# Optimization experiments

Hardware: AMD Instinct MI355X
Metric: run time of the kernel (lower is better)

The kernel has to match this reference:

```python
import jax, jax.numpy as jnp
import numpy as np

WINDOW = 128
LOOK_BACK = 1
LOOK_FWD = 0   # causal=True -> look_forward defaults to 0
DIM = 64       # rotary dim == head dim


def look_around(x, backward=LOOK_BACK, forward=LOOK_FWD, pad_value=-1):
    # x: [b, windows, window, ...]; pad along windows axis, concat along axis 2
    w = x.shape[1]
    pad = [(0, 0), (backward, forward)] + [(0, 0)] * (x.ndim - 2)
    px = jnp.pad(x, pad, constant_values=pad_value)
    return jnp.concatenate([px[:, i:i + w] for i in range(forward + backward + 1)], axis=2)


def rotate_half(x):
    h = (x.shape[-1] + 1) // 2  # ceil split, matches torch .split([ceil, floor])
    x1, x2 = x[..., :h], x[..., h:]
    return jnp.concatenate([-x2, x1], axis=-1)


def setup_inputs() -> dict:
    key = jax.random.key(0)
    kq, kk, kv = jax.random.split(key, 3)
    shape = (4, 16, 4096, 64)
    return {
        "q": jax.random.normal(kq, shape, dtype=jnp.float32),
        "k": jax.random.normal(kk, shape, dtype=jnp.float32),
        "v": jax.random.normal(kv, shape, dtype=jnp.float32),
    }


def reference(q, k, v):
    B, H, T, e = q.shape
    b = B * H
    q, k, v = (t.reshape(b, T, e) for t in (q, k, v))

    # sinusoidal rotary embeddings (start_pos = 0)
    inv_freq = 1.0 / (10000.0 ** (jnp.arange(0, DIM, 2, dtype=jnp.float32) / DIM))
    t_idx = jnp.arange(T, dtype=jnp.float32)
    freqs = jnp.einsum('i,j->ij', t_idx, inv_freq)          # [T, DIM/2]
    emb = jnp.concatenate([freqs, freqs], axis=-1)[:, :DIM][None]  # [1, T, DIM]
    cos, sin = jnp.cos(emb), jnp.sin(emb)
    q = q * cos + rotate_half(q) * sin
    k = k * cos + rotate_half(k) * sin

    # T is a multiple of WINDOW so autopad is a no-op
    w = T // WINDOW
    bq, bk, bv = (t.reshape(b, w, WINDOW, e) for t in (q, k, v))
    bk = look_around(bk)   # [b, w, (LB+LF+1)*WINDOW, e], padded with -1 (masked below)
    bv = look_around(bv)

    b_t = jnp.arange(T).reshape(1, w, WINDOW)
    bq_t = b_t
    bq_k = look_around(b_t)  # [1, w, (LB+LF+1)*WINDOW]

    dots = (jnp.einsum('bwie,bwje->bwij', bq.astype(jnp.float32), bk.astype(jnp.float32))
            * (e ** -0.5)).astype(q.dtype)
    mask_value = -jnp.finfo(dots.dtype).max

    # causal mask (exact_windowsize=False)
    causal_mask = bq_t[:, :, :, None] < bq_k[:, :, None, :]
    dots = jnp.where(causal_mask, mask_value, dots)
    # look-around padding mask
    dots = jnp.where((bq_k == -1)[:, :, None, :], mask_value, dots)

    attn = jax.nn.softmax(dots, axis=-1)
    out = jnp.einsum('bwij,bwje->bwie', attn, bv)
    return out.reshape(B, H, T, e)
```

## Files before the change

### kernel.cpp

```cpp
#include <hip/hip_runtime.h>
#include <hip/hip_bf16.h>

#define T_LEN 4096
#define DHEAD 64
#define WINSZ 128
#define NWIN 32
#define NBH 64
#define NWPB 4
#define NGRP (NWIN / NWPB)
#define FLTMAX 3.402823466e38f

typedef float f32x4 __attribute__((ext_vector_type(4)));
typedef short s16x8 __attribute__((ext_vector_type(8)));
typedef short s16x4 __attribute__((ext_vector_type(4)));

__device__ __forceinline__ unsigned short f2b(float x) {
  return __builtin_bit_cast(unsigned short, __float2bfloat16(x));
}

__global__ void rope_tab_kernel(float* __restrict__ tab) {
  const int idx = blockIdx.x * 256 + threadIdx.x;
  if (idx >= T_LEN * 32) return;
  const int t = idx >> 5;
  const int i = idx & 31;
  const float freq = powf(10000.0f, -(float)i / 32.0f);
  float s, c;
  sincosf((float)t * freq, &s, &c);
  tab[idx] = c;
  tab[T_LEN * 32 + idx] = s;
}

__global__ __launch_bounds__(512, 4) void lattn_kernel(
    const float* __restrict__ qg, const float* __restrict__ kg,
    const float* __restrict__ vg, const float* __restrict__ tab,
    float* __restrict__ outg) {
  __shared__ __align__(16) unsigned short Kh[2][WINSZ * DHEAD];
  __shared__ __align__(16) unsigned short Vh[2][DHEAD * WINSZ];

  const int bid = blockIdx.x;
  const int grp = bid & (NGRP - 1);
  const int bh  = bid >> 3;
  const int tid = threadIdx.x;
  const int lane = tid & 63;
  const int wv = tid >> 6;
  const int l15 = lane & 15;
  const int g = lane >> 4;

  const size_t base = (size_t)bh * T_LEN * DHEAD;
  const int win0 = grp * NWPB;
  const bool use_tab = (tab != nullptr);
  const float* ct = tab;
  const float* st = tab + T_LEN * 32;

  auto stage_half = [&](int hb, int kb) {
    {
      const int c = tid & 7;
      const int rr = tid >> 3;
      #pragma unroll
      for (int p = 0; p < 2; ++p) {
        const int kr = p * 64 + rr;
        const int kt = kb + kr;
        float xa[4] = {0.f,0.f,0.f,0.f}, xb[4] = {0.f,0.f,0.f,0.f};
        float cs[4] = {1.f,1.f,1.f,1.f}, sn[4] = {0.f,0.f,0.f,0.f};
        if (kt >= 0) {
          const float* kp = kg + base + (size_t)kt * DHEAD + 4 * c;
          *(float4*)xa = *(const float4*)kp;
          *(float4*)xb = *(const float4*)(kp + 32);
          if (use_tab) {
            *(float4*)cs = *(const float4*)(ct + kt * 32 + 4 * c);
            *(float4*)sn = *(const float4*)(st + kt * 32 + 4 * c);
          } else {
            #pragma unroll
            for (int j = 0; j < 4; ++j) {
              const float f = powf(10000.0f, -(float)(4 * c + j) / 32.0f);
              sincosf((float)kt * f, &sn[j], &cs[j]);
            }
          }
        }
        unsigned wlo[2], whi[2];
        #pragma unroll
        for (int h = 0; h < 2; ++h) {
          const int j0 = 2 * h, j1 = 2 * h + 1;
          wlo[h] = (unsigned)f2b(xa[j0]*cs[j0] - xb[j0]*sn[j0]) |
                   ((unsigned)f2b(xa[j1]*cs[j1] - xb[j1]*sn[j1]) << 16);
          whi[h] = (unsigned)f2b(xb[j0]*cs[j0] + xa[j0]*sn[j0]) |
                   ((unsigned)f2b(xb[j1]*cs[j1] + xa[j1]*sn[j1]) << 16);
        }
        const int su = (kr & 7) << 3;
        *(uint2*)&Kh[hb][kr * 64 + ((4 * c) ^ su)] = uint2{wlo[0], wlo[1]};
        *(uint2*)&Kh[hb][kr * 64 + ((4 * c + 32) ^ su)] = uint2{whi[0], whi[1]};
      }
    }
    {
      const int c = tid & 15;
      const int rp = tid >> 4;
      #pragma unroll
      for (int p = 0; p < 2; ++p) {
        const int kr = (p * 32 + rp) * 2;
        const int kt = kb + kr;
        float va[4] = {0.f,0.f,0.f,0.f}, vb[4] = {0.f,0.f,0.f,0.f};
        if (kt >= 0)
          *(float4*)va = *(const float4*)(vg + base + (size_t)kt * DHEAD + 4 * c);
        if (kt + 1 >= 0)
          *(float4*)vb = *(const float4*)(vg + base + (size_t)(kt + 1) * DHEAD + 4 * c);
        #pragma unroll
        for (int j = 0; j < 4; ++j) {
          const int d = 4 * c + j;
          const unsigned val = (unsigned)f2b(va[j]) | ((unsigned)f2b(vb[j]) << 16);
          *(unsigned*)&Vh[hb][d * WINSZ + (kr ^ ((d & 15) << 3))] = val;
        }
      }
    }
  };

  stage_half(0, win0 * WINSZ - WINSZ);
  stage_half(1, win0 * WINSZ);

  #pragma unroll 1
  for (int t = 0; t < NWPB; ++t) {
    const int win = win0 + t;
    const int q0 = win * WINSZ;
    const int pb = t & 1, ob = (t + 1) & 1;

    s16x8 qa0, qa1;
    {
      const int qrow = q0 + wv * 16 + l15;
      const float* qp = qg + base + (size_t)qrow * DHEAD + 8 * g;
      float xa[8], xb[8], cs[8], sn[8];
      *(float4*)&xa[0] = *(const float4*)qp;
      *(float4*)&xa[4] = *(const float4*)(qp + 4);
      *(float4*)&xb[0] = *(const float4*)(qp + 32);
      *(float4*)&xb[4] = *(const float4*)(qp + 36);
      if (use_tab) {
        const float* cp = ct + qrow * 32 + 8 * g;
        const float* sp = st + qrow * 32 + 8 * g;
        *(float4*)&cs[0] = *(const float4*)cp;
        *(float4*)&cs[4] = *(const float4*)(cp + 4);
        *(float4*)&sn[0] = *(const float4*)sp;
        *(float4*)&sn[4] = *(const float4*)(sp + 4);
      } else {
        #pragma unroll
        for (int j = 0; j < 8; ++j) {
          const float f = powf(10000.0f, -(float)(8 * g + j) / 32.0f);
          sincosf((float)qrow * f, &sn[j], &cs[j]);
        }
      }
      #pragma unroll
      for (int j = 0; j < 8; ++j) {
        qa0[j] = (short)f2b(xa[j]*cs[j] - xb[j]*sn[j]);
        qa1[j] = (short)f2b(xb[j]*cs[j] + xa[j]*sn[j]);
      }
    }

    __syncthreads();

    s16x8 pa[8];
    float inv;
    {
      f32x4 acc[16];
      #pragma unroll
      for (int nt = 0; nt < 16; ++nt) acc[nt] = f32x4{0.f, 0.f, 0.f, 0.f};
      #pragma unroll
      for (int nt = 0; nt < 16; ++nt) {
        const int hb = (nt < 8) ? pb : ob;
        const int krh = (nt & 7) * 16 + l15;
        const int su = (krh & 7) << 3;
        const s16x8 k0f = *(const s16x8*)&Kh[hb][krh * 64 + ((8 * g) ^ su)];
        const s16x8 k1f = *(const s16x8*)&Kh[hb][krh * 64 + ((8 * g + 32) ^ su)];
        acc[nt] = __builtin_amdgcn_mfma_f32_16x16x32_bf16(k0f, qa0, acc[nt], 0, 0, 0);
        acc[nt] = __builtin_amdgcn_mfma_f32_16x16x32_bf16(k1f, qa1, acc[nt], 0, 0, 0);
      }
      const int qloc = wv * 16 + l15;
      float mx = -FLTMAX;
      #pragma unroll
      for (int nt = 0; nt < 16; ++nt) {
        const bool pad = (win == 0) && (nt < 8);
        #pragma unroll
        for (int r = 0; r < 4; ++r) {
          const int kloc = nt * 16 + 4 * g + r;
          const bool msk = pad || (kloc > WINSZ + qloc);
          const float s = msk ? -FLTMAX : acc[nt][r];
          acc[nt][r] = s;
          mx = fmaxf(mx, s);
        }
      }
      mx = fmaxf(mx, __shfl_xor(mx, 16));
      mx = fmaxf(mx, __shfl_xor(mx, 32));
      float den = 0.f;
      #pragma unroll
      for (int nt = 0; nt < 16; ++nt) {
        #pragma unroll
        for (int r = 0; r < 4; ++r) {
          const float pv = __expf(0.125f * (acc[nt][r] - mx));
          acc[nt][r] = pv;
          den += pv;
        }
      }
      den += __shfl_xor(den, 16);
      den += __shfl_xor(den, 32);
      inv = 1.0f / den;
      #pragma unroll
      for (int ks = 0; ks < 8; ++ks) {
        #pragma unroll
        for (int j = 0; j < 4; ++j) {
          pa[ks][j]     = (short)f2b(acc[2 * ks][j]);
          pa[ks][j + 4] = (short)f2b(acc[2 * ks + 1][j]);
        }
      }
    }

    f32x4 oacc[4];
    #pragma unroll
    for (int nt = 0; nt < 4; ++nt) oacc[nt] = f32x4{0.f, 0.f, 0.f, 0.f};
    #pragma unroll
    for (int ks = 0; ks < 8; ++ks) {
      const int hb = (ks < 4) ? pb : ob;
      const int c1 = (ks & 3) * 32 + 4 * g;
      #pragma unroll
      for (int nt = 0; nt < 4; ++nt) {
        const int d = nt * 16 + l15;
        const int su = (d & 15) << 3;
        const s16x4 v0 = *(const s16x4*)&Vh[hb][d * WINSZ + (c1 ^ su)];
        const s16x4 v1 = *(const s16x4*)&Vh[hb][d * WINSZ + ((c1 + 16) ^ su)];
        const s16x8 vb = __builtin_shufflevector(v0, v1, 0, 1, 2, 3, 4, 5, 6, 7);
        oacc[nt] = __builtin_amdgcn_mfma_f32_16x16x32_bf16(pa[ks], vb, oacc[nt], 0, 0, 0);
      }
    }

    float* op = outg + base;
    #pragma unroll
    for (int r = 0; r < 4; ++r) {
      const float ir = __shfl(inv, 4 * g + r, 64);
      const int qrow = q0 + wv * 16 + 4 * g + r;
      #pragma unroll
      for (int nt = 0; nt < 4; ++nt)
        op[(size_t)qrow * DHEAD + nt * 16 + l15] = oacc[nt][r] * ir;
    }

    if (t + 1 < NWPB) {
      __syncthreads();
      stage_half(t & 1, (win + 1) * WINSZ);
    }
  }
}

extern "C" void kernel_launch(void* const* d_in, const int* in_sizes, int n_in,
                              void* d_out, int out_size, void* d_ws, size_t ws_size,
                              hipStream_t stream) {
  (void)in_sizes; (void)n_in; (void)out_size;
  const float* q = (const float*)d_in[0];
  const float* k = (const float*)d_in[1];
  const float* v = (const float*)d_in[2];
  float* out = (float*)d_out;

  float* tab = nullptr;
  const size_t tab_bytes = (size_t)2 * T_LEN * 32 * sizeof(float);
  if (ws_size >= tab_bytes) {
    tab = (float*)d_ws;
    rope_tab_kernel<<<dim3((T_LEN * 32 + 255) / 256), dim3(256), 0, stream>>>(tab);
  }
  lattn_kernel<<<dim3(NBH * NGRP), dim3(512), 0, stream>>>(q, k, v, tab, out);
}
```

Baseline: 253.7 us.

## Precompute rotated bf16 K/V in workspace and DMA them into LDS per window

Adds a prep kernel that applies rotary embedding to K, converts K and V to swizzled bf16 (V transposed) in a workspace buffer. The attention kernel then runs one window per block and copies K/V tiles straight into LDS with global_load_lds, removing the per-block fp32 load and convert work. The block index is remapped across the grid, and a single-pass fallback kernel handles the case where the workspace is too small. The trade-off is an extra kernel launch and a full extra write and read of bf16 K/V through global memory, in exchange for less fp32 traffic and less compute inside the attention kernel.

```diff
diff --git a/kernel.cpp b/kernel.cpp
--- a/kernel.cpp
+++ b/kernel.cpp
@@ -6,8 +6,6 @@
 #define WINSZ 128
 #define NWIN 32
 #define NBH 64
-#define NWPB 4
-#define NGRP (NWIN / NWPB)
 #define FLTMAX 3.402823466e38f
 
 typedef float f32x4 __attribute__((ext_vector_type(4)));
@@ -16,6 +14,12 @@
 
 __device__ __forceinline__ unsigned short f2b(float x) {
   return __builtin_bit_cast(unsigned short, __float2bfloat16(x));
+}
+
+__device__ __forceinline__ void dma16(const void* g, void* l) {
+  __builtin_amdgcn_global_load_lds(
+      (const __attribute__((address_space(1))) void*)g,
+      (__attribute__((address_space(3))) void*)l, 16, 0, 0);
 }
 
 __global__ void rope_tab_kernel(float* __restrict__ tab) {
@@ -30,16 +34,78 @@
   tab[T_LEN * 32 + idx] = s;
 }
 
-__global__ __launch_bounds__(512, 4) void lattn_kernel(
-    const float* __restrict__ qg, const float* __restrict__ kg,
-    const float* __restrict__ vg, const float* __restrict__ tab,
+__global__ __launch_bounds__(512, 4) void kv_prep_kernel(
+    const float* __restrict__ kg, const float* __restrict__ vg,
+    const float* __restrict__ tab,
+    unsigned short* __restrict__ Kp, unsigned short* __restrict__ Vp) {
+  const int bid = blockIdx.x;
+  const int chunk = bid & 31;
+  const int bh = bid >> 5;
+  const int tid = threadIdx.x;
+  const int kb = chunk * WINSZ;
+  const size_t base = (size_t)bh * T_LEN * DHEAD;
+  const float* ct = tab;
+  const float* st = tab + T_LEN * 32;
+
+  {
+    const int c = tid & 7;
+    const int rr = tid >> 3;
+    #pragma unroll
+    for (int p = 0; p < 2; ++p) {
+      const int kt = kb + p * 64 + rr;
+      const float* kp = kg + base + (size_t)kt * DHEAD + 4 * c;
+      float xa[4], xb[4], cs[4], sn[4];
+      *(float4*)xa = *(const float4*)kp;
+      *(float4*)xb = *(const float4*)(kp + 32);
+      *(float4*)cs = *(const float4*)(ct + kt * 32 + 4 * c);
+      *(float4*)sn = *(const float4*)(st + kt * 32 + 4 * c);
+      unsigned wlo[2], whi[2];
+      #pragma unroll
+      for (int h = 0; h < 2; ++h) {
+        const int j0 = 2 * h, j1 = 2 * h + 1;
+        wlo[h] = (unsigned)f2b(xa[j0]*cs[j0] - xb[j0]*sn[j0]) |
+                 ((unsigned)f2b(xa[j1]*cs[j1] - xb[j1]*sn[j1]) << 16);
+        whi[h] = (unsigned)f2b(xb[j0]*cs[j0] + xa[j0]*sn[j0]) |
+                 ((unsigned)f2b(xb[j1]*cs[j1] + xa[j1]*sn[j1]) << 16);
+      }
+      const int su = (kt & 7) << 3;
+      unsigned short* krow = Kp + base + (size_t)kt * DHEAD;
+      *(uint2*)&krow[(4 * c) ^ su] = uint2{wlo[0], wlo[1]};
+      *(uint2*)&krow[(4 * c + 32) ^ su] = uint2{whi[0], whi[1]};
+    }
+  }
+  {
+    const int c = tid & 15;
+    const int rp = tid >> 4;
+    unsigned short* vb_base = Vp + (size_t)bh * DHEAD * T_LEN;
+    #pragma unroll
+    for (int p = 0; p < 2; ++p) {
+      const int kr = (p * 32 + rp) * 2;
+      const int kt = kb + kr;
+      float va[4], vb[4];
+      *(float4*)va = *(const float4*)(vg + base + (size_t)kt * DHEAD + 4 * c);
+      *(float4*)vb = *(const float4*)(vg + base + (size_t)(kt + 1) * DHEAD + 4 * c);
+      #pragma unroll
+      for (int j = 0; j < 4; ++j) {
+        const int d = 4 * c + j;
+        const unsigned val = (unsigned)f2b(va[j]) | ((unsigned)f2b(vb[j]) << 16);
+        *(unsigned*)&vb_base[(size_t)d * T_LEN + kb + (kr ^ ((d & 15) << 3))] = val;
+      }
+    }
+  }
+}
+
+__global__ __launch_bounds__(512, 4) void lattn2_kernel(
+    const float* __restrict__ qg, const unsigned short* __restrict__ Kp,
+    const unsigned short* __restrict__ Vp, const float* __restrict__ tab,
     float* __restrict__ outg) {
   __shared__ __align__(16) unsigned short Kh[2][WINSZ * DHEAD];
   __shared__ __align__(16) unsigned short Vh[2][DHEAD * WINSZ];
 
-  const int bid = blockIdx.x;
-  const int grp = bid & (NGRP - 1);
-  const int bh  = bid >> 3;
+  const int H = blockIdx.x;
+  const int L = (H & 7) * 256 + (H >> 3);
+  const int win = L & (NWIN - 1);
+  const int bh  = L >> 5;
   const int tid = threadIdx.x;
   const int lane = tid & 63;
   const int wv = tid >> 6;
@@ -47,200 +113,335 @@
   const int g = lane >> 4;
 
   const size_t base = (size_t)bh * T_LEN * DHEAD;
-  const int win0 = grp * NWPB;
+  const int q0 = win * WINSZ;
+  const float* ct = tab;
+  const float* st = tab + T_LEN * 32;
+
+  {
+    const unsigned short* gk = Kp + base + (size_t)q0 * DHEAD;
+    const unsigned short* gv = Vp + (size_t)bh * DHEAD * T_LEN;
+    #pragma unroll
+    for (int i = 0; i < 2; ++i) {
+      const int idx = (wv * 2 + i) * 512 + lane * 8;
+      dma16(gk + idx, &Kh[1][idx]);
+      const int ch = wv * 2 + i;
+      const int d = ch * 4 + (lane >> 4);
+      const int col = (lane & 15) * 8;
+      dma16(gv + (size_t)d * T_LEN + q0 + col, &Vh[1][ch * 512 + lane * 8]);
+    }
+    if (win > 0) {
+      const unsigned short* gkp = Kp + base + (size_t)(q0 - WINSZ) * DHEAD;
+      #pragma unroll
+      for (int i = 0; i < 2; ++i) {
+        const int idx = (wv * 2 + i) * 512 + lane * 8;
+        dma16(gkp + idx, &Kh[0][idx]);
+        const int ch = wv * 2 + i;
+        const int d = ch * 4 + (lane >> 4);
+        const int col = (lane & 15) * 8;
+        dma16(gv + (size_t)d * T_LEN + (q0 - WINSZ) + col, &Vh[0][ch * 512 + lane * 8]);
+      }
+    } else {
+      #pragma unroll
+      for (int i = 0; i < 2; ++i) {
+        *(uint4*)&Kh[0][tid * 16 + i * 8] = uint4{0u, 0u, 0u, 0u};
+        *(uint4*)&Vh[0][tid * 16 + i * 8] = uint4{0u, 0u, 0u, 0u};
+      }
+    }
+  }
+
+  s16x8 qa0, qa1;
+  {
+    const int qrow = q0 + wv * 16 + l15;
+    const float* qp = qg + base + (size_t)qrow * DHEAD + 8 * g;
+    float xa[8], xb[8], cs[8], sn[8];
+    *(float4*)&xa[0] = *(const float4*)qp;
+    *(float4*)&xa[4] = *(const float4*)(qp + 4);
+    *(float4*)&xb[0] = *(const float4*)(qp + 32);
+    *(float4*)&xb[4] = *(const float4*)(qp + 36);
+    const float* cp = ct + qrow * 32 + 8 * g;
+    const float* sp = st + qrow * 32 + 8 * g;
+    *(float4*)&cs[0] = *(const float4*)cp;
+    *(float4*)&cs[4] = *(const float4*)(cp + 4);
+    *(float4*)&sn[0] = *(const float4*)sp;
+    *(float4*)&sn[4] = *(const float4*)(sp + 4);
+    #pragma unroll
+    for (int j = 0; j < 8; ++j) {
+      qa0[j] = (short)f2b(xa[j]*cs[j] - xb[j]*sn[j]);
+      qa1[j] = (short)f2b(xb[j]*cs[j] + xa[j]*sn[j]);
+    }
+  }
+
+  __syncthreads();
+
+  s16x8 pa[8];
+  float inv;
+  {
+    f32x4 acc[16];
+    #pragma unroll
+    for (int nt = 0; nt < 16; ++nt) acc[nt] = f32x4{0.f, 0.f, 0.f, 0.f};
+    #pragma unroll
+    for (int nt = 0; nt < 16; ++nt) {
+      const int hb = nt >> 3;
+      const int krh = (nt & 7) * 16 + l15;
+      const int su = (krh & 7) << 3;
+      const s16x8 k0f = *(const s16x8*)&Kh[hb][krh * 64 + ((8 * g) ^ su)];
+      const s16x8 k1f = *(const s16x8*)&Kh[hb][krh * 64 + ((8 * g + 32) ^ su)];
+      acc[nt] = __builtin_amdgcn_mfma_f32_16x16x32_bf16(k0f, qa0, acc[nt], 0, 0, 0);
+      acc[nt] = __builtin_amdgcn_mfma_f32_16x16x32_bf16(k1f, qa1, acc[nt], 0, 0, 0);
+    }
+    const int qloc = wv * 16 + l15;
+    float mx = -FLTMAX;
+    #pragma unroll
+    for (int nt = 0; nt < 16; ++nt) {
+      const bool pad = (win == 0) && (nt < 8);
+      #pragma unroll
+      for (int r = 0; r < 4; ++r) {
+        const int kloc = nt * 16 + 4 * g + r;
+        const bool msk = pad || (kloc > WINSZ + qloc);
+        const float s = msk ? -FLTMAX : acc[nt][r];
+        acc[nt][r] = s;
+        mx = fmaxf(mx, s);
+      }
+    }
+    mx = fmaxf(mx, __shfl_xor(mx, 16));
+    mx = fmaxf(mx, __shfl_xor(mx, 32));
+    float den = 0.f;
+    #pragma unroll
+    for (int nt = 0; nt < 16; ++nt) {
+      #pragma unroll
+      for (int r = 0; r < 4; ++r) {
+        const float pv = __expf(0.125f * (acc[nt][r] - mx));
+        acc[nt][r] = pv;
+        den += pv;
+      }
+    }
+    den += __shfl_xor(den, 16);
+    den += __shfl_xor(den, 32);
+    inv = 1.0f / den;
+    #pragma unroll
+    for (int ks = 0; ks < 8; ++ks) {
+      #pragma unroll
+      for (int j = 0; j < 4; ++j) {
+        pa[ks][j]     = (short)f2b(acc[2 * ks][j]);
+        pa[ks][j + 4] = (short)f2b(acc[2 * ks + 1][j]);
+      }
+    }
+  }
+
+  f32x4 oacc[4];
+  #pragma unroll
+  for (int nt = 0; nt < 4; ++nt) oacc[nt] = f32x4{0.f, 0.f, 0.f, 0.f};
+  #pragma unroll
+  for (int ks = 0; ks < 8; ++ks) {
+    const int hb = ks >> 2;
+    const int c1 = (ks & 3) * 32 + 4 * g;
+    #pragma unroll
+    for (int nt = 0; nt < 4; ++nt) {
+      const int d = nt * 16 + l15;
+      const int su = (d & 15) << 3;
+      const s16x4 v0 = *(const s16x4*)&Vh[hb][d * WINSZ + (c1 ^ su)];
+      const s16x4 v1 = *(const s16x4*)&Vh[hb][d * WINSZ + ((c1 + 16) ^ su)];
+      const s16x8 vb = __builtin_shufflevector(v0, v1, 0, 1, 2, 3, 4, 5, 6, 7);
+      oacc[nt] = __builtin_amdgcn_mfma_f32_16x16x32_bf16(pa[ks], vb, oacc[nt], 0, 0, 0);
+    }
+  }
+
+  float* op = outg + base;
+  #pragma unroll
+  for (int r = 0; r < 4; ++r) {
+    const float ir = __shfl(inv, 4 * g + r, 64);
+    const int qrow = q0 + wv * 16 + 4 * g + r;
+    #pragma unroll
+    for (int nt = 0; nt < 4; ++nt)
+      op[(size_t)qrow * DHEAD + nt * 16 + l15] = oacc[nt][r] * ir;
+  }
+}
+
+__global__ __launch_bounds__(512, 4) void lattn_fb_kernel(
+    const float* __restrict__ qg, const float* __restrict__ kg,
+    const float* __restrict__ vg, const float* __restrict__ tab,
+    float* __restrict__ outg) {
+  __shared__ __align__(16) unsigned short Kl[256 * DHEAD];
+  __shared__ __align__(16) unsigned short Vt[DHEAD * 256];
+  const int bid = blockIdx.x;
+  const int win = bid & (NWIN - 1);
+  const int bh  = bid >> 5;
+  const int tid = threadIdx.x;
+  const int lane = tid & 63;
+  const int wv = tid >> 6;
+  const int l15 = lane & 15;
+  const int g = lane >> 4;
+  const size_t base = (size_t)bh * T_LEN * DHEAD;
+  const int q0 = win * WINSZ;
+  const int k0 = q0 - WINSZ;
   const bool use_tab = (tab != nullptr);
   const float* ct = tab;
   const float* st = tab + T_LEN * 32;
-
-  auto stage_half = [&](int hb, int kb) {
-    {
-      const int c = tid & 7;
-      const int rr = tid >> 3;
-      #pragma unroll
-      for (int p = 0; p < 2; ++p) {
-        const int kr = p * 64 + rr;
-        const int kt = kb + kr;
-        float xa[4] = {0.f,0.f,0.f,0.f}, xb[4] = {0.f,0.f,0.f,0.f};
-        float cs[4] = {1.f,1.f,1.f,1.f}, sn[4] = {0.f,0.f,0.f,0.f};
-        if (kt >= 0) {
-          const float* kp = kg + base + (size_t)kt * DHEAD + 4 * c;
-          *(float4*)xa = *(const float4*)kp;
-          *(float4*)xb = *(const float4*)(kp + 32);
-          if (use_tab) {
-            *(float4*)cs = *(const float4*)(ct + kt * 32 + 4 * c);
-            *(float4*)sn = *(const float4*)(st + kt * 32 + 4 * c);
-          } else {
-            #pragma unroll
-            for (int j = 0; j < 4; ++j) {
-              const float f = powf(10000.0f, -(float)(4 * c + j) / 32.0f);
-              sincosf((float)kt * f, &sn[j], &cs[j]);
-            }
+  {
+    const int c = tid & 7;
+    const int rr = tid >> 3;
+    #pragma unroll
+    for (int p = 0; p < 4; ++p) {
+      const int kr = p * 64 + rr;
+      const int kt = k0 + kr;
+      float xa[4] = {0.f,0.f,0.f,0.f}, xb[4] = {0.f,0.f,0.f,0.f};
+      float cs[4] = {1.f,1.f,1.f,1.f}, sn[4] = {0.f,0.f,0.f,0.f};
+      if (kt >= 0) {
+        const float* kp = kg + base + (size_t)kt * DHEAD + 4 * c;
+        *(float4*)xa = *(const float4*)kp;
+        *(float4*)xb = *(const float4*)(kp + 32);
+        if (use_tab) {
+          *(float4*)cs = *(const float4*)(ct + kt * 32 + 4 * c);
+          *(float4*)sn = *(const float4*)(st + kt * 32 + 4 * c);
+        } else {
+          #pragma unroll
+          for (int j = 0; j < 4; ++j) {
+            const float f = powf(10000.0f, -(float)(4 * c + j) / 32.0f);
+            sincosf((float)kt * f, &sn[j], &cs[j]);
           }
         }
-        unsigned wlo[2], whi[2];
-        #pragma unroll
-        for (int h = 0; h < 2; ++h) {
-          const int j0 = 2 * h, j1 = 2 * h + 1;
-          wlo[h] = (unsigned)f2b(xa[j0]*cs[j0] - xb[j0]*sn[j0]) |
-                   ((unsigned)f2b(xa[j1]*cs[j1] - xb[j1]*sn[j1]) << 16);
-          whi[h] = (unsigned)f2b(xb[j0]*cs[j0] + xa[j0]*sn[j0]) |
-                   ((unsigned)f2b(xb[j1]*cs[j1] + xa[j1]*sn[j1]) << 16);
-        }
-        const int su = (kr & 7) << 3;
-        *(uint2*)&Kh[hb][kr * 64 + ((4 * c) ^ su)] = uint2{wlo[0], wlo[1]};
-        *(uint2*)&Kh[hb][kr * 64 + ((4 * c + 32) ^ su)] = uint2{whi[0], whi[1]};
-      }
-    }
-    {
-      const int c = tid & 15;
-      const int rp = tid >> 4;
-      #pragma unroll
-      for (int p = 0; p < 2; ++p) {
-        const int kr = (p * 32 + rp) * 2;
-        const int kt = kb + kr;
-        float va[4] = {0.f,0.f,0.f,0.f}, vb[4] = {0.f,0.f,0.f,0.f};
-        if (kt >= 0)
-          *(float4*)va = *(const float4*)(vg + base + (size_t)kt * DHEAD + 4 * c);
-        if (kt + 1 >= 0)
-          *(float4*)vb = *(const float4*)(vg + base + (size_t)(kt + 1) * DHEAD + 4 * c);
-        #pragma unroll
-        for (int j = 0; j < 4; ++j) {
-          const int d = 4 * c + j;
-          const unsigned val = (unsigned)f2b(va[j]) | ((unsigned)f2b(vb[j]) << 16);
-          *(unsigned*)&Vh[hb][d * WINSZ + (kr ^ ((d & 15) << 3))] = val;
-        }
-      }
-    }
-  };
-
-  stage_half(0, win0 * WINSZ - WINSZ);
-  stage_half(1, win0 * WINSZ);
-
-  #pragma unroll 1
-  for (int t = 0; t < NWPB; ++t) {
-    const int win = win0 + t;
-    const int q0 = win * WINSZ;
-    const int pb = t & 1, ob = (t + 1) & 1;
-
-    s16x8 qa0, qa1;
-    {
-      const int qrow = q0 + wv * 16 + l15;
-      const float* qp = qg + base + (size_t)qrow * DHEAD + 8 * g;
-      float xa[8], xb[8], cs[8], sn[8];
-      *(float4*)&xa[0] = *(const float4*)qp;
-      *(float4*)&xa[4] = *(const float4*)(qp + 4);
-      *(float4*)&xb[0] = *(const float4*)(qp + 32);
-      *(float4*)&xb[4] = *(const float4*)(qp + 36);
-      if (use_tab) {
-        const float* cp = ct + qrow * 32 + 8 * g;
-        const float* sp = st + qrow * 32 + 8 * g;
-        *(float4*)&cs[0] = *(const float4*)cp;
-        *(float4*)&cs[4] = *(const float4*)(cp + 4);
-        *(float4*)&sn[0] = *(const float4*)sp;
-        *(float4*)&sn[4] = *(const float4*)(sp + 4);
-      } else {
-        #pragma unroll
-        for (int j = 0; j < 8; ++j) {
-          const float f = powf(10000.0f, -(float)(8 * g + j) / 32.0f);
-          sincosf((float)qrow * f, &sn[j], &cs[j]);
-        }
-      }
+      }
+      unsigned wlo[2], whi[2];
+      #pragma unroll
+      for (int h = 0; h < 2; ++h) {
+        const int j0 = 2 * h, j1 = 2 * h + 1;
+        wlo[h] = (unsigned)f2b(xa[j0]*cs[j0] - xb[j0]*sn[j0]) |
+                 ((unsigned)f2b(xa[j1]*cs[j1] - xb[j1]*sn[j1]) << 16);
+        whi[h] = (unsigned)f2b(xb[j0]*cs[j0] + xa[j0]*sn[j0]) |
+                 ((unsigned)f2b(xb[j1]*cs[j1] + xa[j1]*sn[j1]) << 16);
+      }
+      const int su = (kr & 7) << 3;
+      *(uint2*)&Kl[kr * 64 + ((4 * c) ^ su)] = uint2{wlo[0], wlo[1]};
+      *(uint2*)&Kl[kr * 64 + ((4 * c + 32) ^ su)] = uint2{whi[0], whi[1]};
+    }
+  }
+  {
+    const int c = tid & 15;
+    const int rp = tid >> 4;
+    #pragma unroll
+    for (int p = 0; p < 4; ++p) {
+      const int kr = (p * 32 + rp) * 2;
+      const int kt = k0 + kr;
+      float va[4] = {0.f,0.f,0.f,0.f}, vb[4] = {0.f,0.f,0.f,0.f};
+      if (kt >= 0)
+        *(float4*)va = *(const float4*)(vg + base + (size_t)kt * DHEAD + 4 * c);
+      if (kt + 1 >= 0)
+        *(float4*)vb = *(const float4*)(vg + base + (size_t)(kt + 1) * DHEAD + 4 * c);
+      #pragma unroll
+      for (int j = 0; j < 4; ++j) {
+        const int d = 4 * c + j;
+        const unsigned val = (unsigned)f2b(va[j]) | ((unsigned)f2b(vb[j]) << 16);
+        *(unsigned*)&Vt[d * 256 + (kr ^ ((d & 7) << 3))] = val;
+      }
+    }
+  }
+  s16x8 qa0, qa1;
+  {
+    const int qrow = q0 + wv * 16 + l15;
+    const float* qp = qg + base + (size_t)qrow * DHEAD + 8 * g;
+    float xa[8], xb[8], cs[8], sn[8];
+    *(float4*)&xa[0] = *(const float4*)qp;
+    *(float4*)&xa[4] = *(const float4*)(qp + 4);
+    *(float4*)&xb[0] = *(const float4*)(qp + 32);
+    *(float4*)&xb[4] = *(const float4*)(qp + 36);
+    if (use_tab) {
+      const float* cp = ct + qrow * 32 + 8 * g;
+      const float* sp = st + qrow * 32 + 8 * g;
+      *(float4*)&cs[0] = *(const float4*)cp;
+      *(float4*)&cs[4] = *(const float4*)(cp + 4);
+      *(float4*)&sn[0] = *(const float4*)sp;
+      *(float4*)&sn[4] = *(const float4*)(sp + 4);
+    } else {
       #pragma unroll
       for (int j = 0; j < 8; ++j) {
-        qa0[j] = (short)f2b(xa[j]*cs[j] - xb[j]*sn[j]);
-        qa1[j] = (short)f2b(xb[j]*cs[j] + xa[j]*sn[j]);
-      }
-    }
-
-    __syncthreads();
-
-    s16x8 pa[8];
-    float inv;
-    {
-      f32x4 acc[16];
-      #pragma unroll
-      for (int nt = 0; nt < 16; ++nt) acc[nt] = f32x4{0.f, 0.f, 0.f, 0.f};
-      #pragma unroll
-      for (int nt = 0; nt < 16; ++nt) {
-        const int hb = (nt < 8) ? pb : ob;
-        const int krh = (nt & 7) * 16 + l15;
-        const int su = (krh & 7) << 3;
-        const s16x8 k0f = *(const s16x8*)&Kh[hb][krh * 64 + ((8 * g) ^ su)];
-        const s16x8 k1f = *(const s16x8*)&Kh[hb][krh * 64 + ((8 * g + 32) ^ su)];
-        acc[nt] = __builtin_amdgcn_mfma_f32_16x16x32_bf16(k0f, qa0, acc[nt], 0, 0, 0);
-        acc[nt] = __builtin_amdgcn_mfma_f32_16x16x32_bf16(k1f, qa1, acc[nt], 0, 0, 0);
-      }
-      const int qloc = wv * 16 + l15;
-      float mx = -FLTMAX;
-      #pragma unroll
-      for (int nt = 0; nt < 16; ++nt) {
-        const bool pad = (win == 0) && (nt < 8);
-        #pragma unroll
-        for (int r = 0; r < 4; ++r) {
-          const int kloc = nt * 16 + 4 * g + r;
-          const bool msk = pad || (kloc > WINSZ + qloc);
-          const float s = msk ? -FLTMAX : acc[nt][r];
-          acc[nt][r] = s;
-          mx = fmaxf(mx, s);
-        }
-      }
-      mx = fmaxf(mx, __shfl_xor(mx, 16));
-      mx = fmaxf(mx, __shfl_xor(mx, 32));
-      float den = 0.f;
-      #pragma unroll
-      for (int nt = 0; nt < 16; ++nt) {
-        #pragma unroll
-        for (int r = 0; r < 4; ++r) {
-          const float pv = __expf(0.125f * (acc[nt][r] - mx));
-          acc[nt][r] = pv;
-          den += pv;
-        }
-      }
-      den += __shfl_xor(den, 16);
-      den += __shfl_xor(den, 32);
-      inv = 1.0f / den;
-      #pragma unroll
-      for (int ks = 0; ks < 8; ++ks) {
-        #pragma unroll
-        for (int j = 0; j < 4; ++j) {
-          pa[ks][j]     = (short)f2b(acc[2 * ks][j]);
-          pa[ks][j + 4] = (short)f2b(acc[2 * ks + 1][j]);
-        }
-      }
-    }
-
-    f32x4 oacc[4];
-    #pragma unroll
-    for (int nt = 0; nt < 4; ++nt) oacc[nt] = f32x4{0.f, 0.f, 0.f, 0.f};
+        const float f = powf(10000.0f, -(float)(8 * g + j) / 32.0f);
+        sincosf((float)qrow * f, &sn[j], &cs[j]);
+      }
+    }
+    #pragma unroll
+    for (int j = 0; j < 8; ++j) {
+      qa0[j] = (short)f2b(xa[j]*cs[j] - xb[j]*sn[j]);
+      qa1[j] = (short)f2b(xb[j]*cs[j] + xa[j]*sn[j]);
+    }
+  }
+  __syncthreads();
+  s16x8 pa[8];
+  float inv;
+  {
+    f32x4 acc[16];
+    #pragma unroll
+    for (int nt = 0; nt < 16; ++nt) acc[nt] = f32x4{0.f, 0.f, 0.f, 0.f};
+    #pragma unroll
+    for (int nt = 0; nt < 16; ++nt) {
+      const int krow = nt * 16 + l15;
+      const int su = (krow & 7) << 3;
+      const s16x8 k0f = *(const s16x8*)&Kl[krow * 64 + ((8 * g) ^ su)];
+      const s16x8 k1f = *(const s16x8*)&Kl[krow * 64 + ((8 * g + 32) ^ su)];
+      acc[nt] = __builtin_amdgcn_mfma_f32_16x16x32_bf16(k0f, qa0, acc[nt], 0, 0, 0);
+      acc[nt] = __builtin_amdgcn_mfma_f32_16x16x32_bf16(k1f, qa1, acc[nt], 0, 0, 0);
+    }
+    const int qloc = wv * 16 + l15;
+    float mx = -FLTMAX;
+    #pragma unroll
+    for (int nt = 0; nt < 16; ++nt) {
+      const bool pad = (win == 0) && (nt < 8);
+      #pragma unroll
+      for (int r = 0; r < 4; ++r) {
+        const int kloc = nt * 16 + 4 * g + r;
+        const bool msk = pad || (kloc > WINSZ + qloc);
+        const float s = msk ? -FLTMAX : acc[nt][r];
+        acc[nt][r] = s;
+        mx = fmaxf(mx, s);
+      }
+    }
+    mx = fmaxf(mx, __shfl_xor(mx, 16));
+    mx = fmaxf(mx, __shfl_xor(mx, 32));
+    float den = 0.f;
+    #pragma unroll
+    for (int nt = 0; nt < 16; ++nt) {
+      #pragma unroll
+      for (int r = 0; r < 4; ++r) {
+        const float pv = __expf(0.125f * (acc[nt][r] - mx));
+        acc[nt][r] = pv;
+        den += pv;
+      }
+    }
+    den += __shfl_xor(den, 16);
+    den += __shfl_xor(den, 32);
+    inv = 1.0f / den;
     #pragma unroll
     for (int ks = 0; ks < 8; ++ks) {
-      const int hb = (ks < 4) ? pb : ob;
-      const int c1 = (ks & 3) * 32 + 4 * g;
-      #pragma unroll
-      for (int nt = 0; nt < 4; ++nt) {
-        const int d = nt * 16 + l15;
-        const int su = (d & 15) << 3;
-        const s16x4 v0 = *(const s16x4*)&Vh[hb][d * WINSZ + (c1 ^ su)];
-        const s16x4 v1 = *(const s16x4*)&Vh[hb][d * WINSZ + ((c1 + 16) ^ su)];
-        const s16x8 vb = __builtin_shufflevector(v0, v1, 0, 1, 2, 3, 4, 5, 6, 7);
-        oacc[nt] = __builtin_amdgcn_mfma_f32_16x16x32_bf16(pa[ks], vb, oacc[nt], 0, 0, 0);
-      }
-    }
-
-    float* op = outg + base;
-    #pragma unroll
-    for (int r = 0; r < 4; ++r) {
-      const float ir = __shfl(inv, 4 * g + r, 64);
-      const int qrow = q0 + wv * 16 + 4 * g + r;
-      #pragma unroll
-      for (int nt = 0; nt < 4; ++nt)
-        op[(size_t)qrow * DHEAD + nt * 16 + l15] = oacc[nt][r] * ir;
-    }
-
-    if (t + 1 < NWPB) {
-      __syncthreads();
-      stage_half(t & 1, (win + 1) * WINSZ);
-    }
+      #pragma unroll
+      for (int j = 0; j < 4; ++j) {
+        pa[ks][j]     = (short)f2b(acc[2 * ks][j]);
+        pa[ks][j + 4] = (short)f2b(acc[2 * ks + 1][j]);
+      }
+    }
+  }
+  f32x4 oacc[4];
+  #pragma unroll
+  for (int nt = 0; nt < 4; ++nt) oacc[nt] = f32x4{0.f, 0.f, 0.f, 0.f};
+  #pragma unroll
+  for (int ks = 0; ks < 8; ++ks) {
+    #pragma unroll
+    for (int nt = 0; nt < 4; ++nt) {
+      const int d = nt * 16 + l15;
+      const int su = (d & 7) << 3;
+      const int c1 = ks * 32 + 4 * g;
+      const s16x4 v0 = *(const s16x4*)&Vt[d * 256 + (c1 ^ su)];
+      const s16x4 v1 = *(const s16x4*)&Vt[d * 256 + ((c1 + 16) ^ su)];
+      const s16x8 vb = __builtin_shufflevector(v0, v1, 0, 1, 2, 3, 4, 5, 6, 7);
+      oacc[nt] = __builtin_amdgcn_mfma_f32_16x16x32_bf16(pa[ks], vb, oacc[nt], 0, 0, 0);
+    }
+  }
+  float* op = outg + base;
+  #pragma unroll
+  for (int r = 0; r < 4; ++r) {
+    const float ir = __shfl(inv, 4 * g + r, 64);
+    const int qrow = q0 + wv * 16 + 4 * g + r;
+    #pragma unroll
+    for (int nt = 0; nt < 4; ++nt)
+      op[(size_t)qrow * DHEAD + nt * 16 + l15] = oacc[nt][r] * ir;
   }
 }
 
@@ -253,11 +454,22 @@
   const float* v = (const float*)d_in[2];
   float* out = (float*)d_out;
 
-  float* tab = nullptr;
   const size_t tab_bytes = (size_t)2 * T_LEN * 32 * sizeof(float);
-  if (ws_size >= tab_bytes) {
-    tab = (float*)d_ws;
+  const size_t kp_bytes  = (size_t)NBH * T_LEN * DHEAD * sizeof(short);
+  const size_t need = tab_bytes + 2 * kp_bytes;
+
+  if (ws_size >= need) {
+    float* tab = (float*)d_ws;
+    unsigned short* Kp = (unsigned short*)((char*)d_ws + tab_bytes);
+    unsigned short* Vp = (unsigned short*)((char*)d_ws + tab_bytes + kp_bytes);
     rope_tab_kernel<<<dim3((T_LEN * 32 + 255) / 256), dim3(256), 0, stream>>>(tab);
-  }
-  lattn_kernel<<<dim3(NBH * NGRP), dim3(512), 0, stream>>>(q, k, v, tab, out);
-}
+    kv_prep_kernel<<<dim3(NBH * NWIN), dim3(512), 0, stream>>>(k, v, tab, Kp, Vp);
+    lattn2_kernel<<<dim3(NBH * NWIN), dim3(512), 0, stream>>>(q, Kp, Vp, tab, out);
+  } else if (ws_size >= tab_bytes) {
+    float* tab = (float*)d_ws;
+    rope_tab_kernel<<<dim3((T_LEN * 32 + 255) / 256), dim3(256), 0, stream>>>(tab);
+    lattn_fb_kernel<<<dim3(NBH * NWIN), dim3(512), 0, stream>>>(q, k, v, tab, out);
+  } else {
+    lattn_fb_kernel<<<dim3(NBH * NWIN), dim3(512), 0, stream>>>(q, k, v, nullptr, out);
+  }
+}
```

New measurement: 261.5 us. 3.1% more time.
